# Kernel tuning notes

Hardware: AMD Instinct MI355X
Metric: run time of the kernel (lower is better)

The kernel has to match this reference:

```python
import jax, jax.numpy as jnp
import numpy as np

S, B, H = 8192, 32, 256

def setup_inputs() -> dict:
    key = jax.random.key(0)
    k1, k2 = jax.random.split(key)
    enc_output_i = jax.random.normal(k1, (S, B, H), dtype=jnp.float32)
    enc_or_dec_hid_i = jax.random.normal(k2, (1, B, H), dtype=jnp.float32)
    return {"enc_output_i": enc_output_i, "enc_or_dec_hid_i": enc_or_dec_hid_i}

def reference(enc_output_i, enc_or_dec_hid_i):
    # enc_output_i: [S, B, H]; enc_or_dec_hid_i: [1, B, H]
    hid = enc_or_dec_hid_i[0]                              # [B, H]
    scores = jnp.einsum('sbh,bh->bs', enc_output_i, hid)   # [B, S]
    weights = jax.nn.softmax(scores, axis=1)               # [B, S]
    context = jnp.einsum('sbh,bs->bh', enc_output_i, weights)  # [B, H]
    return context
```

## Files before the change

kernel.cpp:

```cpp
#include <hip/hip_runtime.h>

#define S_DIM 8192
#define B_DIM 32
#define H_DIM 256
#define CH 64
#define ROWS_PER_CHUNK (S_DIM / CH)
#define WAVES 4
#define GROUPS 4
#define RPI (WAVES * GROUPS)
#define ITERS (ROWS_PER_CHUNK / RPI)
#define SHIFT 40.0f

typedef float f32x4 __attribute__((ext_vector_type(4)));

__global__ __launch_bounds__(256, 4) void attn_partial(
    const float* __restrict__ enc, const float* __restrict__ hid,
    float* __restrict__ ws_acc, float* __restrict__ ws_l)
{
    const int b     = blockIdx.x;
    const int chunk = blockIdx.y;
    const int tid   = threadIdx.x;
    const int w     = tid >> 6;
    const int lane  = tid & 63;
    const int g     = lane >> 4;
    const int t     = lane & 15;
    const int grp   = (w << 2) | g;

    f32x4 hf[4];
    #pragma unroll
    for (int j = 0; j < 4; j++)
        hf[j] = *(const f32x4*)(hid + b * H_DIM + j * 64 + t * 4);

    float l = 0.f;
    f32x4 acc[4];
    #pragma unroll
    for (int j = 0; j < 4; j++) acc[j] = (f32x4){0.f, 0.f, 0.f, 0.f};

    const int s0 = chunk * ROWS_PER_CHUNK + grp;
    const float* rowp = enc + (size_t)s0 * (B_DIM * H_DIM) + b * H_DIM + t * 4;

    for (int i = 0; i < ITERS; i++) {
        const float* row = rowp + (size_t)i * RPI * (B_DIM * H_DIM);
        f32x4 a[4];
        #pragma unroll
        for (int j = 0; j < 4; j++)
            a[j] = __builtin_nontemporal_load((const f32x4*)(row + j * 64));

        float d = 0.f;
        #pragma unroll
        for (int j = 0; j < 4; j++) {
            d = fmaf(a[j].x, hf[j].x, d);
            d = fmaf(a[j].y, hf[j].y, d);
            d = fmaf(a[j].z, hf[j].z, d);
            d = fmaf(a[j].w, hf[j].w, d);
        }
        #pragma unroll
        for (int off = 8; off >= 1; off >>= 1)
            d += __shfl_xor(d, off, 64);

        const float p = __expf(d - SHIFT);
        l += p;
        #pragma unroll
        for (int j = 0; j < 4; j++) {
            acc[j].x = fmaf(p, a[j].x, acc[j].x);
            acc[j].y = fmaf(p, a[j].y, acc[j].y);
            acc[j].z = fmaf(p, a[j].z, acc[j].z);
            acc[j].w = fmaf(p, a[j].w, acc[j].w);
        }
    }

    __shared__ float lds_acc[RPI][H_DIM];
    __shared__ float lds_l[RPI];
    #pragma unroll
    for (int j = 0; j < 4; j++)
        *(f32x4*)&lds_acc[grp][j * 64 + t * 4] = acc[j];
    if (t == 0) lds_l[grp] = l;
    __syncthreads();

    const int h = tid;
    float cb = 0.f;
    #pragma unroll
    for (int q = 0; q < RPI; q++) cb += lds_acc[q][h];
    ws_acc[((size_t)b * CH + chunk) * H_DIM + h] = cb;
    if (tid == 0) {
        float ls = 0.f;
        #pragma unroll
        for (int q = 0; q < RPI; q++) ls += lds_l[q];
        ws_l[b * CH + chunk] = ls;
    }
}

__global__ __launch_bounds__(1024) void attn_final(
    const float* __restrict__ ws_acc, const float* __restrict__ ws_l,
    float* __restrict__ out)
{
    const int b   = blockIdx.x;
    const int tid = threadIdx.x;
    const int h   = tid & (H_DIM - 1);
    const int qr  = tid >> 8;
    __shared__ float Ls;
    __shared__ float part[4][H_DIM];

    if (tid < CH) {
        float lp = ws_l[b * CH + tid];
        #pragma unroll
        for (int off = 32; off >= 1; off >>= 1)
            lp += __shfl_xor(lp, off, 64);
        if (tid == 0) Ls = lp;
    }

    float s = 0.f;
    const float* base = ws_acc + (size_t)b * CH * H_DIM + h;
    #pragma unroll
    for (int c = 0; c < CH / 4; c++)
        s += base[(size_t)(c * 4 + qr) * H_DIM];
    part[qr][h] = s;
    __syncthreads();

    if (tid < H_DIM) {
        float tot = part[0][h] + part[1][h] + part[2][h] + part[3][h];
        out[b * H_DIM + h] = tot / Ls;
    }
}

extern "C" void kernel_launch(void* const* d_in, const int* in_sizes, int n_in,
                              void* d_out, int out_size, void* d_ws, size_t ws_size,
                              hipStream_t stream) {
    const float* enc = (const float*)d_in[0];
    const float* hid = (const float*)d_in[1];
    float* ws_acc = (float*)d_ws;
    float* ws_l   = ws_acc + (size_t)B_DIM * CH * H_DIM;
    float* out = (float*)d_out;

    attn_partial<<<dim3(B_DIM, CH), 256, 0, stream>>>(enc, hid, ws_acc, ws_l);
    attn_final<<<B_DIM, 1024, 0, stream>>>(ws_acc, ws_l, out);
}
```

Baseline: 341.1 us.

## Fuse final reduction into partial kernel via last-block atomic counter

Replaces the separate final-reduction kernel with a last-block-done pattern. Each block publishes its partial results, fences, and atomically increments a per-batch counter, and the block that arrives last sums the 64 chunk partials and writes the output. This removes one kernel launch and its launch gap, but adds a memset launch for the counters, an atomic per block, and a serial 64-step reduction done by a single block per batch.

```diff
diff --git a/kernel.cpp b/kernel.cpp
--- a/kernel.cpp
+++ b/kernel.cpp
@@ -13,9 +13,10 @@
 
 typedef float f32x4 __attribute__((ext_vector_type(4)));
 
-__global__ __launch_bounds__(256, 4) void attn_partial(
+__global__ __launch_bounds__(256, 4) void attn_fused(
     const float* __restrict__ enc, const float* __restrict__ hid,
-    float* __restrict__ ws_acc, float* __restrict__ ws_l)
+    float* __restrict__ ws_acc, float* __restrict__ ws_l,
+    int* __restrict__ cnt, float* __restrict__ out)
 {
     const int b     = blockIdx.x;
     const int chunk = blockIdx.y;
@@ -88,39 +89,35 @@
         for (int q = 0; q < RPI; q++) ls += lds_l[q];
         ws_l[b * CH + chunk] = ls;
     }
-}
 
-__global__ __launch_bounds__(1024) void attn_final(
-    const float* __restrict__ ws_acc, const float* __restrict__ ws_l,
-    float* __restrict__ out)
-{
-    const int b   = blockIdx.x;
-    const int tid = threadIdx.x;
-    const int h   = tid & (H_DIM - 1);
-    const int qr  = tid >> 8;
+    __threadfence();
+    __shared__ int lastFlag;
+    if (tid == 0) {
+        int old = __hip_atomic_fetch_add(&cnt[b], 1, __ATOMIC_ACQ_REL,
+                                         __HIP_MEMORY_SCOPE_AGENT);
+        lastFlag = (old == CH - 1);
+    }
+    __syncthreads();
+    if (!lastFlag) return;
+
     __shared__ float Ls;
-    __shared__ float part[4][H_DIM];
-
     if (tid < CH) {
-        float lp = ws_l[b * CH + tid];
+        float lp = __hip_atomic_load(&ws_l[b * CH + tid], __ATOMIC_RELAXED,
+                                     __HIP_MEMORY_SCOPE_AGENT);
         #pragma unroll
         for (int off = 32; off >= 1; off >>= 1)
             lp += __shfl_xor(lp, off, 64);
         if (tid == 0) Ls = lp;
     }
+    __syncthreads();
 
     float s = 0.f;
     const float* base = ws_acc + (size_t)b * CH * H_DIM + h;
-    #pragma unroll
-    for (int c = 0; c < CH / 4; c++)
-        s += base[(size_t)(c * 4 + qr) * H_DIM];
-    part[qr][h] = s;
-    __syncthreads();
-
-    if (tid < H_DIM) {
-        float tot = part[0][h] + part[1][h] + part[2][h] + part[3][h];
-        out[b * H_DIM + h] = tot / Ls;
-    }
+    #pragma unroll 8
+    for (int c = 0; c < CH; c++)
+        s += __hip_atomic_load(&base[(size_t)c * H_DIM], __ATOMIC_RELAXED,
+                               __HIP_MEMORY_SCOPE_AGENT);
+    out[b * H_DIM + h] = s / Ls;
 }
 
 extern "C" void kernel_launch(void* const* d_in, const int* in_sizes, int n_in,
@@ -130,8 +127,9 @@
     const float* hid = (const float*)d_in[1];
     float* ws_acc = (float*)d_ws;
     float* ws_l   = ws_acc + (size_t)B_DIM * CH * H_DIM;
+    int*   cnt    = (int*)(ws_l + B_DIM * CH);
     float* out = (float*)d_out;
 
-    attn_partial<<<dim3(B_DIM, CH), 256, 0, stream>>>(enc, hid, ws_acc, ws_l);
-    attn_final<<<B_DIM, 1024, 0, stream>>>(ws_acc, ws_l, out);
+    hipMemsetAsync(cnt, 0, B_DIM * sizeof(int), stream);
+    attn_fused<<<dim3(B_DIM, CH), 256, 0, stream>>>(enc, hid, ws_acc, ws_l, cnt, out);
 }
```

Result: slower. 819.8 us (+140.4%).
